# Kernel optimization log

Measured on AMD Instinct MI355X. Metric: run time of the kernel, lower is better.

## Reference

```python
import jax, jax.numpy as jnp
import numpy as np
import math

B, L, H, N2, NB = 16, 1024, 256, 64, 6
IN_DIM, OUT_DIM, STEP_EMB, NFEAT = 1, 1, 128, 4


def setup_inputs() -> dict:
    key = jax.random.key(0)
    ks = jax.random.split(key, 20)
    def rn(k, shape, s=0.02):
        return jax.random.normal(k, shape, dtype=jnp.float32) * s
    inp = {}
    inp["input"] = jax.random.normal(ks[0], (B, L, IN_DIM), dtype=jnp.float32)
    inp["t"] = jax.random.uniform(ks[1], (B,), dtype=jnp.float32) * 1000.0  # diffusion steps
    inp["features"] = jax.random.normal(ks[2], (B, L, NFEAT), dtype=jnp.float32)
    # input_init / time_init / output head (Linear weights stored (in,out))
    inp["W_in"] = rn(ks[3], (IN_DIM, H)); inp["b_in"] = jnp.zeros((H,), jnp.float32)
    inp["W_t1"] = rn(ks[4], (STEP_EMB, H)); inp["b_t1"] = jnp.zeros((H,), jnp.float32)
    inp["W_t2"] = rn(ks[5], (H, H)); inp["b_t2"] = jnp.zeros((H,), jnp.float32)
    inp["Wh1"] = rn(ks[6], (H, H)); inp["bh1"] = jnp.zeros((H,), jnp.float32)
    inp["Wh2"] = rn(ks[7], (H, OUT_DIM)); inp["bh2"] = jnp.zeros((OUT_DIM,), jnp.float32)
    # per-block params, stacked on leading NB axis
    inp["ln_g"] = jnp.ones((NB, H), jnp.float32); inp["ln_b"] = jnp.zeros((NB, H), jnp.float32)
    lo, hi = math.log(0.001), math.log(0.1)
    inp["log_dt"] = jax.random.uniform(ks[8], (NB, H), dtype=jnp.float32) * (hi - lo) + lo
    inp["A_re"] = 0.5 * jnp.ones((NB, H, N2), jnp.float32)  # A = -A_re + i*A_im (S4D-Lin)
    inp["A_im"] = jnp.broadcast_to(math.pi * jnp.arange(N2, dtype=jnp.float32), (NB, H, N2)) * jnp.ones((NB, H, N2), jnp.float32)
    inp["C_re"] = rn(ks[9], (NB, 2, H, N2), 0.7071)  # 2 = bidirectional channels
    inp["C_im"] = rn(ks[10], (NB, 2, H, N2), 0.7071)
    inp["D"] = rn(ks[11], (NB, H), 1.0)
    inp["Wo_s4"] = rn(ks[12], (NB, H, H)); inp["bo_s4"] = jnp.zeros((NB, H), jnp.float32)
    inp["Wt"] = rn(ks[13], (NB, H, H)); inp["bt"] = jnp.zeros((NB, H), jnp.float32)
    inp["W1"] = rn(ks[14], (NB, H, H)); inp["b1"] = jnp.zeros((NB, H), jnp.float32)
    inp["W2"] = rn(ks[15], (NB, H, H)); inp["b2"] = jnp.zeros((NB, H), jnp.float32)
    inp["Wf"] = rn(ks[16], (NB, NFEAT, H)); inp["bf"] = jnp.zeros((NB, H), jnp.float32)
    return inp


def _layernorm_ch(x, g, b, eps=1e-5):
    # x: (B,H,L); LayerNorm over channel dim H (torch applies it on (B,L,H))
    mu = x.mean(1, keepdims=True)
    v = ((x - mu) ** 2).mean(1, keepdims=True)
    return (x - mu) * jax.lax.rsqrt(v + eps) * g[None, :, None] + b[None, :, None]


def _s4(z, log_dt, A_re, A_im, C_re, C_im, D, Wo, bo):
    # Diagonal SSM (S4D) bidirectional convolution. z: (B,H,L)
    Lz = z.shape[-1]
    dt = jnp.exp(log_dt)                      # (H,)
    A = jax.lax.complex(-A_re, A_im)          # (H,N2)
    dtA = dt[:, None] * A                     # (H,N2)
    C = jax.lax.complex(C_re, C_im)           # (2,H,N2)
    Bt = C * (jnp.exp(dtA) - 1.0) / A         # ZOH discretization
    vand = jnp.exp(dtA[:, :, None] * jnp.arange(Lz, dtype=jnp.float32))  # (H,N2,L)
    K = 2.0 * jnp.real(jnp.einsum('chn,hnl->chl', Bt, vand))             # (2,H,L)
    zpad = jnp.zeros_like(K[0])
    k = jnp.concatenate([K[0], zpad], -1) + jnp.concatenate([zpad, K[1][:, ::-1]], -1)  # (H,2L)
    y = jnp.fft.irfft(jnp.fft.rfft(z, n=2 * Lz) * jnp.fft.rfft(k, n=2 * Lz), n=2 * Lz)[..., :Lz]
    y = y + z * D[:, None]
    y = jax.nn.gelu(y, approximate=False)
    return jnp.einsum('bhl,ho->bol', y, Wo) + bo[None, :, None]


def reference(input, t, features, W_in, b_in, W_t1, b_t1, W_t2, b_t2, Wh1, bh1, Wh2, bh2,
              ln_g, ln_b, log_dt, A_re, A_im, C_re, C_im, D, Wo_s4, bo_s4,
              Wt, bt, W1, b1, W2, b2, Wf, bf):
    x = jax.nn.relu(input @ W_in + b_in)                       # (B,L,H)
    half = W_t1.shape[0] // 2
    freqs = jnp.exp(jnp.arange(half, dtype=jnp.float32) * (-math.log(10000.0) / (half - 1)))
    ang = t[:, None] * freqs[None, :]
    temb = jnp.concatenate([jnp.sin(ang), jnp.cos(ang)], -1)   # (B,step_emb)
    temb = jax.nn.silu(temb @ W_t1 + b_t1)
    temb = jax.nn.silu(temb @ W_t2 + b_t2)                     # (B,H)
    x = jnp.swapaxes(x, 1, 2)                                  # (B,H,L)
    feat = jnp.swapaxes(features, 1, 2)                        # (B,F,L)
    skip = jnp.zeros_like(x)
    nb = ln_g.shape[0]
    for i in range(nb):
        tb = (temb @ Wt[i] + bt[i])[:, :, None]                # time_linear, broadcast over L
        u = x + tb
        z = _layernorm_ch(u, ln_g[i], ln_b[i])
        z = _s4(z, log_dt[i], A_re[i], A_im[i], C_re[i], C_im[i], D[i], Wo_s4[i], bo_s4[i])
        out = z + u                                            # S4Layer residual
        out = out + jnp.einsum('bfl,fh->bhl', feat, Wf[i]) + bf[i][None, :, None]
        g = jnp.tanh(out) * jax.nn.sigmoid(out)                # gated activation
        x = jnp.einsum('bhl,ho->bol', g, W1[i]) + b1[i][None, :, None] + x
        skip = skip + jnp.einsum('bhl,ho->bol', g, W2[i]) + b2[i][None, :, None]
    skip = jnp.swapaxes(skip, 1, 2)                            # (B,L,H)
    h = jax.nn.relu(skip @ Wh1 + bh1)
    return h @ Wh2 + bh2 + input
```

## Files before the change

kernel.cpp:

```cpp
#include <hip/hip_runtime.h>
#include <cmath>

constexpr int cB = 16, cL = 1024, cH = 256, cN = 64, cNB = 6, cNF = 4;
constexpr int cC = 8, cLc = cL / cC;
constexpr size_t SZ = (size_t)cB * cH * cL;

__global__ __launch_bounds__(256) void temb_kernel(
    const float* __restrict__ t, const float* __restrict__ Wt1, const float* __restrict__ bt1,
    const float* __restrict__ Wt2, const float* __restrict__ bt2,
    const float* __restrict__ Wt, const float* __restrict__ btb, float* __restrict__ tb) {
  __shared__ float e0[128], h1[256], h2[256];
  int b = blockIdx.x, tid = threadIdx.x;
  if (tid < 64) {
    float fr = expf((float)tid * (-logf(10000.0f) / 63.0f));
    float ang = t[b] * fr;
    e0[tid] = sinf(ang);
    e0[tid + 64] = cosf(ang);
  }
  __syncthreads();
  float a = bt1[tid];
  for (int k = 0; k < 128; ++k) a = fmaf(e0[k], Wt1[k * cH + tid], a);
  h1[tid] = a / (1.0f + expf(-a));
  __syncthreads();
  a = bt2[tid];
  for (int k = 0; k < 256; ++k) a = fmaf(h1[k], Wt2[k * cH + tid], a);
  h2[tid] = a / (1.0f + expf(-a));
  __syncthreads();
  for (int i = 0; i < cNB; ++i) {
    float acc = btb[i * cH + tid];
    const float* w = Wt + (size_t)i * cH * cH;
    for (int k = 0; k < 256; ++k) acc = fmaf(h2[k], w[k * cH + tid], acc);
    tb[((size_t)i * cB + b) * cH + tid] = acc;
  }
}

__global__ __launch_bounds__(256) void init_kernel(const float* __restrict__ inp,
    const float* __restrict__ Win, const float* __restrict__ bin,
    float* __restrict__ x, float* __restrict__ skip) {
  int idx = blockIdx.x * 256 + threadIdx.x;
  int l = idx & (cL - 1);
  int h = (idx >> 10) & (cH - 1);
  int b = idx >> 18;
  float v = fmaf(inp[b * cL + l], Win[h], bin[h]);
  x[idx] = v > 0.0f ? v : 0.0f;
  skip[idx] = 0.0f;
}

__global__ __launch_bounds__(256) void pre_ln_kernel(const float* __restrict__ x,
    const float* __restrict__ tb_all, const float* __restrict__ ln_g, const float* __restrict__ ln_b,
    float* __restrict__ z, int blk) {
  __shared__ float red[8][64];
  __shared__ float mur[64], rsr[64];
  int b = blockIdx.x >> 4;
  int l0 = (blockIdx.x & 15) << 6;
  int lq = threadIdx.x & 63, hq = threadIdx.x >> 6;
  int l = l0 + lq;
  const float* tb = tb_all + ((size_t)blk * cB + b) * cH;
  size_t base = ((size_t)b * cH + hq * 64) * cL + l;
  float s = 0.0f, s2 = 0.0f;
  for (int hh = 0; hh < 64; ++hh) {
    float v = x[base + (size_t)hh * cL] + tb[hq * 64 + hh];
    s += v;
    s2 = fmaf(v, v, s2);
  }
  red[hq][lq] = s;
  red[4 + hq][lq] = s2;
  __syncthreads();
  if (hq == 0) {
    float st = red[0][lq] + red[1][lq] + red[2][lq] + red[3][lq];
    float s2t = red[4][lq] + red[5][lq] + red[6][lq] + red[7][lq];
    float mu = st * (1.0f / cH);
    float var = s2t * (1.0f / cH) - mu * mu;
    mur[lq] = mu;
    rsr[lq] = rsqrtf(var + 1e-5f);
  }
  __syncthreads();
  float mu = mur[lq], r = rsr[lq];
  const float* g = ln_g + blk * cH;
  const float* be = ln_b + blk * cH;
  for (int hh = 0; hh < 64; ++hh) {
    int h = hq * 64 + hh;
    float v = (x[base + (size_t)hh * cL] + tb[h] - mu) * r;
    z[base + (size_t)hh * cL] = fmaf(v, g[h], be[h]);
  }
}

__global__ __launch_bounds__(256) void s4param_kernel(
    const float* __restrict__ logdt, const float* __restrict__ Are, const float* __restrict__ Aim,
    const float* __restrict__ Cre, const float* __restrict__ Cim,
    float4* __restrict__ P, float2* __restrict__ PW, int blk) {
  int idx = blockIdx.x * 256 + threadIdx.x;
  int n = idx & (cN - 1);
  int h = (idx >> 6) & (cH - 1);
  int dir = idx >> 14;
  float dt = expf(logdt[blk * cH + h]);
  float are = Are[((size_t)blk * cH + h) * cN + n];
  float aim = Aim[((size_t)blk * cH + h) * cN + n];
  float e = expf(-dt * are);
  float sn, cs;
  sincosf(dt * aim, &sn, &cs);
  float wr = e * cs, wi = e * sn;
  float inv = 1.0f / (are * are + aim * aim);
  float xr = wr - 1.0f, xi = wi;
  float tr = (xi * aim - xr * are) * inv;
  float ti = (-xr * aim - xi * are) * inv;
  float cr = Cre[(((size_t)blk * 2 + dir) * cH + h) * cN + n];
  float ci = Cim[(((size_t)blk * 2 + dir) * cH + h) * cN + n];
  float br = 2.0f * (cr * tr - ci * ti);
  float bi = 2.0f * (cr * ti + ci * tr);
  P[idx] = make_float4(wr, wi, br, bi);
  if (dir == 0) {
    float rr = wr, ri = wi;
#pragma unroll
    for (int q = 0; q < 7; ++q) {
      float nr = rr * rr - ri * ri;
      ri = 2.0f * rr * ri;
      rr = nr;
    }
    PW[h * cN + n] = make_float2(rr, ri);
  }
}

__global__ __launch_bounds__(256) void scanA1_kernel(const float* __restrict__ zb,
    const float4* __restrict__ P, float2* __restrict__ E) {
  int c = blockIdx.x, bh = blockIdx.y, dir = blockIdx.z;
  int b = bh >> 3, h0 = (bh & 7) << 5;
  int tid = threadIdx.x, wv = tid >> 6, lane = tid & 63;
  int hs = lane >> 3, j = lane & 7;
  int h = h0 + wv * 8 + hs;
  float wr[8], wi[8], sr[8], si[8];
  const float4* Ph = P + ((size_t)dir * cH + h) * cN + j * 8;
#pragma unroll
  for (int k = 0; k < 8; ++k) {
    float4 p4 = Ph[k];
    wr[k] = p4.x; wi[k] = p4.y;
    sr[k] = 0.0f; si[k] = 0.0f;
  }
  const float* zr = zb + ((size_t)b * cH + h) * cL;
  int c0 = c * cLc;
  if (dir == 0) {
    for (int m = 0; m < cLc / 4; ++m) {
      float4 z4 = *(const float4*)&zr[c0 + (m << 2)];
#pragma unroll
      for (int q = 0; q < 4; ++q) {
        float zv = q == 0 ? z4.x : q == 1 ? z4.y : q == 2 ? z4.z : z4.w;
#pragma unroll
        for (int k = 0; k < 8; ++k) {
          float nr = fmaf(wr[k], sr[k], zv);
          nr = fmaf(-wi[k], si[k], nr);
          float ni = wr[k] * si[k];
          ni = fmaf(wi[k], sr[k], ni);
          sr[k] = nr; si[k] = ni;
        }
      }
    }
  } else {
    for (int m = cLc / 4 - 1; m >= 0; --m) {
      float4 z4 = *(const float4*)&zr[c0 + (m << 2)];
#pragma unroll
      for (int q = 3; q >= 0; --q) {
        float zv = q == 0 ? z4.x : q == 1 ? z4.y : q == 2 ? z4.z : z4.w;
#pragma unroll
        for (int k = 0; k < 8; ++k) {
          float nr = fmaf(wr[k], sr[k], zv);
          nr = fmaf(-wi[k], si[k], nr);
          float ni = wr[k] * si[k];
          ni = fmaf(wi[k], sr[k], ni);
          sr[k] = nr; si[k] = ni;
        }
      }
    }
  }
  float2* Eo = E + ((((size_t)dir * cC + c) * cB + b) * cH + h) * cN + j * 8;
#pragma unroll
  for (int k = 0; k < 8; ++k) Eo[k] = make_float2(sr[k], si[k]);
}

__global__ __launch_bounds__(256) void scanA2_kernel(const float* __restrict__ zb,
    const float4* __restrict__ P, const float2* __restrict__ PW, const float2* __restrict__ E,
    float* __restrict__ yf, float* __restrict__ ybk) {
  int c = blockIdx.x, bh = blockIdx.y, dir = blockIdx.z;
  int b = bh >> 3, h0 = (bh & 7) << 5;
  int tid = threadIdx.x, wv = tid >> 6, lane = tid & 63;
  int hs = lane >> 3, j = lane & 7;
  int h = h0 + wv * 8 + hs;
  float sr[8] = {}, si[8] = {};
  {
    float qr[8], qi[8];
    const float2* PWh = PW + (size_t)h * cN + j * 8;
#pragma unroll
    for (int k = 0; k < 8; ++k) {
      float2 q2 = PWh[k];
      qr[k] = q2.x; qi[k] = q2.y;
    }
    const size_t cstride = (size_t)cB * cH * cN;
    const float2* Eb = E + (((size_t)dir * cC * cB + b) * cH + h) * cN + j * 8;
    if (dir == 0) {
      for (int cc = 0; cc < c; ++cc) {
        const float2* Ec = Eb + cc * cstride;
#pragma unroll
        for (int k = 0; k < 8; ++k) {
          float2 e2 = Ec[k];
          float t_r = fmaf(qr[k], sr[k], e2.x);
          t_r = fmaf(-qi[k], si[k], t_r);
          float t_i = fmaf(qr[k], si[k], e2.y);
          t_i = fmaf(qi[k], sr[k], t_i);
          sr[k] = t_r; si[k] = t_i;
        }
      }
    } else {
      for (int cc = cC - 1; cc > c; --cc) {
        const float2* Ec = Eb + cc * cstride;
#pragma unroll
        for (int k = 0; k < 8; ++k) {
          float2 e2 = Ec[k];
          float t_r = fmaf(qr[k], sr[k], e2.x);
          t_r = fmaf(-qi[k], si[k], t_r);
          float t_i = fmaf(qr[k], si[k], e2.y);
          t_i = fmaf(qi[k], sr[k], t_i);
          sr[k] = t_r; si[k] = t_i;
        }
      }
    }
  }
  float wr[8], wi[8], br[8], bi[8];
  const float4* Ph = P + ((size_t)dir * cH + h) * cN + j * 8;
#pragma unroll
  for (int k = 0; k < 8; ++k) {
    float4 p4 = Ph[k];
    wr[k] = p4.x; wi[k] = p4.y; br[k] = p4.z; bi[k] = p4.w;
  }
  const float* zr = zb + ((size_t)b * cH + h) * cL;
  int c0 = c * cLc;
  if (dir == 0) {
    float* yr = yf + ((size_t)b * cH + h) * cL;
    for (int m = 0; m < cLc / 4; ++m) {
      float4 z4 = *(const float4*)&zr[c0 + (m << 2)];
#pragma unroll
      for (int q = 0; q < 4; ++q) {
        float zv = q == 0 ? z4.x : q == 1 ? z4.y : q == 2 ? z4.z : z4.w;
        float p = 0.0f;
#pragma unroll
        for (int k = 0; k < 8; ++k) {
          float nr = fmaf(wr[k], sr[k], zv);
          nr = fmaf(-wi[k], si[k], nr);
          float ni = wr[k] * si[k];
          ni = fmaf(wi[k], sr[k], ni);
          sr[k] = nr; si[k] = ni;
          p = fmaf(br[k], nr, p);
          p = fmaf(-bi[k], ni, p);
        }
        p += __shfl_xor(p, 1);
        p += __shfl_xor(p, 2);
        p += __shfl_xor(p, 4);
        if (j == 0) yr[c0 + (m << 2) + q] = p;
      }
    }
  } else {
    float* yr = ybk + ((size_t)b * cH + h) * cL;
    for (int m = cLc / 4 - 1; m >= 0; --m) {
      float4 z4 = *(const float4*)&zr[c0 + (m << 2)];
#pragma unroll
      for (int q = 3; q >= 0; --q) {
        float zv = q == 0 ? z4.x : q == 1 ? z4.y : q == 2 ? z4.z : z4.w;
        float p = 0.0f;
#pragma unroll
        for (int k = 0; k < 8; ++k) {
          p = fmaf(br[k], sr[k], p);
          p = fmaf(-bi[k], si[k], p);
        }
        p += __shfl_xor(p, 1);
        p += __shfl_xor(p, 2);
        p += __shfl_xor(p, 4);
        if (j == 0) yr[c0 + (m << 2) + q] = p;
#pragma unroll
        for (int k = 0; k < 8; ++k) {
          float nr = fmaf(wr[k], sr[k], zv);
          nr = fmaf(-wi[k], si[k], nr);
          float ni = wr[k] * si[k];
          ni = fmaf(wi[k], sr[k], ni);
          sr[k] = nr; si[k] = ni;
        }
      }
    }
  }
}

__global__ __launch_bounds__(256) void scan_kernel(
    const float* __restrict__ zb, const float* __restrict__ log_dt,
    const float* __restrict__ A_re, const float* __restrict__ A_im,
    const float* __restrict__ C_re, const float* __restrict__ C_im,
    float* __restrict__ yf, float* __restrict__ ybk, int blk) {
  int dir = blockIdx.y;
  int b = blockIdx.x >> 3;
  int h0 = (blockIdx.x & 7) << 5;
  int tid = threadIdx.x;
  int wv = tid >> 6, lane = tid & 63;
  int hs = lane >> 3, j = lane & 7;
  int h = h0 + wv * 8 + hs;
  float dt = expf(log_dt[blk * cH + h]);
  const float* Ar = A_re + ((size_t)blk * cH + h) * cN;
  const float* Ai = A_im + ((size_t)blk * cH + h) * cN;
  const float* Cr = C_re + (((size_t)blk * 2 + dir) * cH + h) * cN;
  const float* Ci = C_im + (((size_t)blk * 2 + dir) * cH + h) * cN;
  float wr[8], wi[8], br[8], bi[8], sr[8], si[8];
#pragma unroll
  for (int k = 0; k < 8; ++k) {
    int n = j * 8 + k;
    float are = Ar[n], aim = Ai[n];
    float e = expf(-dt * are);
    float sn, cs;
    sincosf(dt * aim, &sn, &cs);
    float w_r = e * cs, w_i = e * sn;
    float inv = 1.0f / (are * are + aim * aim);
    float xr = w_r - 1.0f, xi = w_i;
    float tr = (xi * aim - xr * are) * inv;
    float ti = (-xr * aim - xi * are) * inv;
    float cr = Cr[n], ci = Ci[n];
    br[k] = 2.0f * (cr * tr - ci * ti);
    bi[k] = 2.0f * (cr * ti + ci * tr);
    wr[k] = w_r; wi[k] = w_i;
    sr[k] = 0.0f; si[k] = 0.0f;
  }
  const float* zr = zb + ((size_t)b * cH + h) * cL;
  if (dir == 0) {
    float* yr = yf + ((size_t)b * cH + h) * cL;
    for (int l = 0; l < cL; ++l) {
      float zv = zr[l];
      float p = 0.0f;
#pragma unroll
      for (int k = 0; k < 8; ++k) {
        float nr = fmaf(wr[k], sr[k], zv);
        nr = fmaf(-wi[k], si[k], nr);
        float ni = wr[k] * si[k];
        ni = fmaf(wi[k], sr[k], ni);
        sr[k] = nr; si[k] = ni;
        p = fmaf(br[k], nr, p);
        p = fmaf(-bi[k], ni, p);
      }
      p += __shfl_xor(p, 1);
      p += __shfl_xor(p, 2);
      p += __shfl_xor(p, 4);
      if (j == 0) yr[l] = p;
    }
  } else {
    float* yr = ybk + ((size_t)b * cH + h) * cL;
    for (int l = cL - 1; l >= 0; --l) {
      float p = 0.0f;
#pragma unroll
      for (int k = 0; k < 8; ++k) {
        p = fmaf(br[k], sr[k], p);
        p = fmaf(-bi[k], si[k], p);
      }
      p += __shfl_xor(p, 1);
      p += __shfl_xor(p, 2);
      p += __shfl_xor(p, 4);
      if (j == 0) yr[l] = p;
      float zv = zr[l];
#pragma unroll
      for (int k = 0; k < 8; ++k) {
        float nr = fmaf(wr[k], sr[k], zv);
        nr = fmaf(-wi[k], si[k], nr);
        float ni = wr[k] * si[k];
        ni = fmaf(wi[k], sr[k], ni);
        sr[k] = nr; si[k] = ni;
      }
    }
  }
}

__global__ __launch_bounds__(256) void gelu_kernel(const float* __restrict__ y2,
    const float* __restrict__ zz, const float* __restrict__ Dp, float* __restrict__ y1io, int blk) {
  int idx = blockIdx.x * 256 + threadIdx.x;
  int h = (idx >> 10) & (cH - 1);
  float v = y1io[idx] + y2[idx] + zz[idx] * Dp[blk * cH + h];
  y1io[idx] = 0.5f * v * (1.0f + erff(v * 0.70710678118654752f));
}

#define GEMM_CORE(WPTR)                                                          \
  int l0 = blockIdx.x * 128, o0 = blockIdx.y * 64, b = blockIdx.z;               \
  int tid = threadIdx.x;                                                         \
  int tx = tid & 15, ty = tid >> 4;                                              \
  const float* Gb = G + (size_t)b * cH * cL;                                     \
  float acc[4][8] = {};                                                          \
  {                                                                              \
    int ar = tid >> 6, ac = tid & 63;                                            \
    int brr = tid >> 7, bc = tid & 127;                                          \
    for (int kk = 0; kk < cH; kk += 16) {                                        \
      _Pragma("unroll")                                                          \
      for (int rr = 0; rr < 4; ++rr)                                             \
        As[ar + rr * 4][ac] = (WPTR)[(size_t)(kk + ar + rr * 4) * cH + o0 + ac]; \
      _Pragma("unroll")                                                          \
      for (int rr = 0; rr < 8; ++rr)                                             \
        Bs[brr + rr * 2][bc] = Gb[(size_t)(kk + brr + rr * 2) * cL + l0 + bc];   \
      __syncthreads();                                                           \
      _Pragma("unroll")                                                          \
      for (int k = 0; k < 16; ++k) {                                             \
        const float4 av = *(const float4*)&As[k][ty << 2];                       \
        const float4 b0 = *(const float4*)&Bs[k][tx << 3];                       \
        const float4 b1 = *(const float4*)&Bs[k][(tx << 3) + 4];                 \
        FMA8(0, av.x) FMA8(1, av.y) FMA8(2, av.z) FMA8(3, av.w)                  \
      }                                                                          \
      __syncthreads();                                                           \
    }                                                                            \
  }

#define FMA8(oi, aw)                                     \
  acc[oi][0] = fmaf(aw, b0.x, acc[oi][0]);               \
  acc[oi][1] = fmaf(aw, b0.y, acc[oi][1]);               \
  acc[oi][2] = fmaf(aw, b0.z, acc[oi][2]);               \
  acc[oi][3] = fmaf(aw, b0.w, acc[oi][3]);               \
  acc[oi][4] = fmaf(aw, b1.x, acc[oi][4]);               \
  acc[oi][5] = fmaf(aw, b1.y, acc[oi][5]);               \
  acc[oi][6] = fmaf(aw, b1.z, acc[oi][6]);               \
  acc[oi][7] = fmaf(aw, b1.w, acc[oi][7]);

__global__ __launch_bounds__(256) void gemm_act_kernel(const float* __restrict__ W,
    const float* __restrict__ bo, const float* __restrict__ G,
    const float* __restrict__ x, const float* __restrict__ tb_all,
    const float* __restrict__ features, const float* __restrict__ Wf,
    const float* __restrict__ bfb, float* __restrict__ C, int blk) {
  __shared__ float As[16][64];
  __shared__ float Bs[16][128];
  GEMM_CORE(W)
  int lbase = l0 + (tx << 3);
  float4 fv[8];
#pragma unroll
  for (int li = 0; li < 8; ++li)
    fv[li] = *(const float4*)&features[((size_t)b * cL + lbase + li) * cNF];
  const float* Wfi = Wf + (size_t)blk * cNF * cH;
  const float* tb = tb_all + ((size_t)blk * cB + b) * cH;
#pragma unroll
  for (int oi = 0; oi < 4; ++oi) {
    int oo = o0 + (ty << 2) + oi;
    float wf0 = Wfi[oo], wf1 = Wfi[cH + oo], wf2 = Wfi[2 * cH + oo], wf3 = Wfi[3 * cH + oo];
    float bb = bo[oo] + bfb[blk * cH + oo] + tb[oo];
    size_t row = ((size_t)b * cH + oo) * cL + lbase;
    const float4 x0 = *(const float4*)&x[row];
    const float4 x1 = *(const float4*)&x[row + 4];
    float xv[8] = {x0.x, x0.y, x0.z, x0.w, x1.x, x1.y, x1.z, x1.w};
    float out[8];
#pragma unroll
    for (int li = 0; li < 8; ++li) {
      float v = acc[oi][li] + bb + xv[li];
      v = fmaf(fv[li].x, wf0, v);
      v = fmaf(fv[li].y, wf1, v);
      v = fmaf(fv[li].z, wf2, v);
      v = fmaf(fv[li].w, wf3, v);
      float tv = tanhf(v);
      float sv = 1.0f / (1.0f + expf(-v));
      out[li] = tv * sv;
    }
    *(float4*)&C[row] = make_float4(out[0], out[1], out[2], out[3]);
    *(float4*)&C[row + 4] = make_float4(out[4], out[5], out[6], out[7]);
  }
}

__global__ __launch_bounds__(256) void gemm_dual_kernel(const float* __restrict__ W1,
    const float* __restrict__ b1, const float* __restrict__ W2, const float* __restrict__ b2,
    const float* __restrict__ G, float* __restrict__ xio, float* __restrict__ skio) {
  __shared__ float As[16][64];
  __shared__ float As2[16][64];
  __shared__ float Bs[16][128];
  int l0 = blockIdx.x * 128, o0 = blockIdx.y * 64, b = blockIdx.z;
  int tid = threadIdx.x;
  int tx = tid & 15, ty = tid >> 4;
  const float* Gb = G + (size_t)b * cH * cL;
  float acc[4][8] = {};
  float acc2[4][8] = {};
  {
    int ar = tid >> 6, ac = tid & 63;
    int brr = tid >> 7, bc = tid & 127;
    for (int kk = 0; kk < cH; kk += 16) {
#pragma unroll
      for (int rr = 0; rr < 4; ++rr) {
        As[ar + rr * 4][ac] = W1[(size_t)(kk + ar + rr * 4) * cH + o0 + ac];
        As2[ar + rr * 4][ac] = W2[(size_t)(kk + ar + rr * 4) * cH + o0 + ac];
      }
#pragma unroll
      for (int rr = 0; rr < 8; ++rr)
        Bs[brr + rr * 2][bc] = Gb[(size_t)(kk + brr + rr * 2) * cL + l0 + bc];
      __syncthreads();
#pragma unroll
      for (int k = 0; k < 16; ++k) {
        const float4 b0 = *(const float4*)&Bs[k][tx << 3];
        const float4 b1v = *(const float4*)&Bs[k][(tx << 3) + 4];
        {
          const float4 av = *(const float4*)&As[k][ty << 2];
#define FMA8D(AC, oi, aw)                          \
  AC[oi][0] = fmaf(aw, b0.x, AC[oi][0]);           \
  AC[oi][1] = fmaf(aw, b0.y, AC[oi][1]);           \
  AC[oi][2] = fmaf(aw, b0.z, AC[oi][2]);           \
  AC[oi][3] = fmaf(aw, b0.w, AC[oi][3]);           \
  AC[oi][4] = fmaf(aw, b1v.x, AC[oi][4]);          \
  AC[oi][5] = fmaf(aw, b1v.y, AC[oi][5]);          \
  AC[oi][6] = fmaf(aw, b1v.z, AC[oi][6]);          \
  AC[oi][7] = fmaf(aw, b1v.w, AC[oi][7]);
          FMA8D(acc, 0, av.x) FMA8D(acc, 1, av.y) FMA8D(acc, 2, av.z) FMA8D(acc, 3, av.w)
        }
        {
          const float4 av = *(const float4*)&As2[k][ty << 2];
          FMA8D(acc2, 0, av.x) FMA8D(acc2, 1, av.y) FMA8D(acc2, 2, av.z) FMA8D(acc2, 3, av.w)
        }
      }
      __syncthreads();
    }
  }
  int lbase = l0 + (tx << 3);
#pragma unroll
  for (int oi = 0; oi < 4; ++oi) {
    int oo = o0 + (ty << 2) + oi;
    float bb1 = b1[oo], bb2 = b2[oo];
    size_t row = ((size_t)b * cH + oo) * cL + lbase;
    float4 xv0 = *(const float4*)&xio[row];
    float4 xv1 = *(const float4*)&xio[row + 4];
    float4 sv0 = *(const float4*)&skio[row];
    float4 sv1 = *(const float4*)&skio[row + 4];
    xv0.x += acc[oi][0] + bb1; xv0.y += acc[oi][1] + bb1;
    xv0.z += acc[oi][2] + bb1; xv0.w += acc[oi][3] + bb1;
    xv1.x += acc[oi][4] + bb1; xv1.y += acc[oi][5] + bb1;
    xv1.z += acc[oi][6] + bb1; xv1.w += acc[oi][7] + bb1;
    sv0.x += acc2[oi][0] + bb2; sv0.y += acc2[oi][1] + bb2;
    sv0.z += acc2[oi][2] + bb2; sv0.w += acc2[oi][3] + bb2;
    sv1.x += acc2[oi][4] + bb2; sv1.y += acc2[oi][5] + bb2;
    sv1.z += acc2[oi][6] + bb2; sv1.w += acc2[oi][7] + bb2;
    *(float4*)&xio[row] = xv0;
    *(float4*)&xio[row + 4] = xv1;
    *(float4*)&skio[row] = sv0;
    *(float4*)&skio[row + 4] = sv1;
  }
}

__global__ __launch_bounds__(256) void gemm_relu_kernel(const float* __restrict__ W,
    const float* __restrict__ bias, const float* __restrict__ G, float* __restrict__ C) {
  __shared__ float As[16][64];
  __shared__ float Bs[16][128];
  GEMM_CORE(W)
  int lbase = l0 + (tx << 3);
#pragma unroll
  for (int oi = 0; oi < 4; ++oi) {
    int oo = o0 + (ty << 2) + oi;
    float bb = bias[oo];
    size_t row = ((size_t)b * cH + oo) * cL + lbase;
    float4 v0, v1;
    v0.x = fmaxf(acc[oi][0] + bb, 0.0f); v0.y = fmaxf(acc[oi][1] + bb, 0.0f);
    v0.z = fmaxf(acc[oi][2] + bb, 0.0f); v0.w = fmaxf(acc[oi][3] + bb, 0.0f);
    v1.x = fmaxf(acc[oi][4] + bb, 0.0f); v1.y = fmaxf(acc[oi][5] + bb, 0.0f);
    v1.z = fmaxf(acc[oi][6] + bb, 0.0f); v1.w = fmaxf(acc[oi][7] + bb, 0.0f);
    *(float4*)&C[row] = v0;
    *(float4*)&C[row + 4] = v1;
  }
}

__global__ __launch_bounds__(256) void head_kernel(const float* __restrict__ hb,
    const float* __restrict__ Wh2, const float* __restrict__ bh2,
    const float* __restrict__ inp, float* __restrict__ out) {
  int idx = blockIdx.x * 256 + threadIdx.x;
  int b = idx >> 10, l = idx & (cL - 1);
  float acc = bh2[0] + inp[idx];
  const float* hr = hb + (size_t)b * cH * cL + l;
  for (int o = 0; o < cH; ++o) acc = fmaf(hr[(size_t)o * cL], Wh2[o], acc);
  out[idx] = acc;
}

extern "C" void kernel_launch(void* const* d_in, const int* in_sizes, int n_in,
                              void* d_out, int out_size, void* d_ws, size_t ws_size,
                              hipStream_t stream) {
  const float* input = (const float*)d_in[0];
  const float* t     = (const float*)d_in[1];
  const float* feats = (const float*)d_in[2];
  const float* W_in  = (const float*)d_in[3];
  const float* b_in  = (const float*)d_in[4];
  const float* W_t1  = (const float*)d_in[5];
  const float* b_t1  = (const float*)d_in[6];
  const float* W_t2  = (const float*)d_in[7];
  const float* b_t2  = (const float*)d_in[8];
  const float* Wh1   = (const float*)d_in[9];
  const float* bh1   = (const float*)d_in[10];
  const float* Wh2   = (const float*)d_in[11];
  const float* bh2   = (const float*)d_in[12];
  const float* ln_g  = (const float*)d_in[13];
  const float* ln_b  = (const float*)d_in[14];
  const float* logdt = (const float*)d_in[15];
  const float* A_re  = (const float*)d_in[16];
  const float* A_im  = (const float*)d_in[17];
  const float* C_re  = (const float*)d_in[18];
  const float* C_im  = (const float*)d_in[19];
  const float* Dp    = (const float*)d_in[20];
  const float* Wo_s4 = (const float*)d_in[21];
  const float* bo_s4 = (const float*)d_in[22];
  const float* Wt    = (const float*)d_in[23];
  const float* bt_   = (const float*)d_in[24];
  const float* W1    = (const float*)d_in[25];
  const float* b1    = (const float*)d_in[26];
  const float* W2    = (const float*)d_in[27];
  const float* b2    = (const float*)d_in[28];
  const float* Wf    = (const float*)d_in[29];
  const float* bf_   = (const float*)d_in[30];

  float* ws = (float*)d_ws;
  float* xb   = ws;
  float* skb  = ws + SZ;
  float* zbuf = ws + 2 * SZ;
  float* yb   = ws + 3 * SZ;
  float* y2b  = ws + 4 * SZ;
  float* tbb  = ws + 5 * SZ;
  size_t off = 5 * SZ + 32768;
  float4* Pbuf = (float4*)(ws + off);
  float2* PWb  = (float2*)(ws + off + 131072);
  float2* Ebuf = (float2*)(ws + off + 131072 + 32768);
  const size_t NEED = (off + 131072 + 32768 + (size_t)2 * cC * cB * cH * cN * 2) * 4;
  const bool chunked = ws_size >= NEED;

  dim3 ggrid(cL / 128, cH / 64, cB);
  dim3 sgrid(cC, cB * (cH / 32), 2);

  temb_kernel<<<cB, 256, 0, stream>>>(t, W_t1, b_t1, W_t2, b_t2, Wt, bt_, tbb);
  init_kernel<<<(int)(SZ / 256), 256, 0, stream>>>(input, W_in, b_in, xb, skb);

  for (int i = 0; i < cNB; ++i) {
    pre_ln_kernel<<<cB * (cL / 64), 256, 0, stream>>>(xb, tbb, ln_g, ln_b, zbuf, i);
    if (chunked) {
      s4param_kernel<<<128, 256, 0, stream>>>(logdt, A_re, A_im, C_re, C_im, Pbuf, PWb, i);
      scanA1_kernel<<<sgrid, 256, 0, stream>>>(zbuf, Pbuf, Ebuf);
      scanA2_kernel<<<sgrid, 256, 0, stream>>>(zbuf, Pbuf, PWb, Ebuf, yb, y2b);
    } else {
      scan_kernel<<<dim3(cB * (cH / 32), 2), 256, 0, stream>>>(zbuf, logdt, A_re, A_im, C_re, C_im, yb, y2b, i);
    }
    gelu_kernel<<<(int)(SZ / 256), 256, 0, stream>>>(y2b, zbuf, Dp, yb, i);
    gemm_act_kernel<<<ggrid, 256, 0, stream>>>(
        Wo_s4 + (size_t)i * cH * cH, bo_s4 + i * cH, yb, xb, tbb, feats, Wf, bf_, zbuf, i);
    gemm_dual_kernel<<<ggrid, 256, 0, stream>>>(
        W1 + (size_t)i * cH * cH, b1 + i * cH, W2 + (size_t)i * cH * cH, b2 + i * cH,
        zbuf, xb, skb);
  }

  gemm_relu_kernel<<<ggrid, 256, 0, stream>>>(Wh1, bh1, skb, yb);
  head_kernel<<<(cB * cL) / 256, 256, 0, stream>>>(yb, Wh2, bh2, input, (float*)d_out);
}
```

Measured before the change: 1.942 ms.

## Fuse bidirectional scan passes, add inter-chunk carry kernel, fold D-skip and GELU into scan

Each scan kernel now handles both directions in one block instead of splitting them over a grid z-dimension. A new scanB kernel propagates chunk carries once and stores exclusive prefix states in place, so scanA2 no longer recomputes the serial chunk recurrence per chunk. scanA2 adds both directions' outputs in LDS, applies the D skip term and GELU, and writes y directly, which removes the y2 buffer and the separate gelu kernel. In exchange there are half as many scan blocks (less parallelism), an extra small kernel launch, and more LDS use per block.

```diff
diff --git a/kernel.cpp b/kernel.cpp
--- a/kernel.cpp
+++ b/kernel.cpp
@@ -4,6 +4,10 @@
 constexpr int cB = 16, cL = 1024, cH = 256, cN = 64, cNB = 6, cNF = 4;
 constexpr int cC = 8, cLc = cL / cC;
 constexpr size_t SZ = (size_t)cB * cH * cL;
+
+__device__ __forceinline__ float gelu_f(float v) {
+  return 0.5f * v * (1.0f + erff(v * 0.70710678118654752f));
+}
 
 __global__ __launch_bounds__(256) void temb_kernel(
     const float* __restrict__ t, const float* __restrict__ Wt1, const float* __restrict__ bt1,
@@ -123,22 +127,18 @@
 
 __global__ __launch_bounds__(256) void scanA1_kernel(const float* __restrict__ zb,
     const float4* __restrict__ P, float2* __restrict__ E) {
-  int c = blockIdx.x, bh = blockIdx.y, dir = blockIdx.z;
+  int c = blockIdx.x, bh = blockIdx.y;
   int b = bh >> 3, h0 = (bh & 7) << 5;
   int tid = threadIdx.x, wv = tid >> 6, lane = tid & 63;
   int hs = lane >> 3, j = lane & 7;
   int h = h0 + wv * 8 + hs;
-  float wr[8], wi[8], sr[8], si[8];
-  const float4* Ph = P + ((size_t)dir * cH + h) * cN + j * 8;
-#pragma unroll
-  for (int k = 0; k < 8; ++k) {
-    float4 p4 = Ph[k];
-    wr[k] = p4.x; wi[k] = p4.y;
-    sr[k] = 0.0f; si[k] = 0.0f;
-  }
   const float* zr = zb + ((size_t)b * cH + h) * cL;
   int c0 = c * cLc;
-  if (dir == 0) {
+  {
+    float wr[8], wi[8], sr[8] = {}, si[8] = {};
+    const float4* Ph = P + (size_t)h * cN + j * 8;
+#pragma unroll
+    for (int k = 0; k < 8; ++k) { float4 p4 = Ph[k]; wr[k] = p4.x; wi[k] = p4.y; }
     for (int m = 0; m < cLc / 4; ++m) {
       float4 z4 = *(const float4*)&zr[c0 + (m << 2)];
 #pragma unroll
@@ -154,7 +154,15 @@
         }
       }
     }
-  } else {
+    float2* Eo = E + ((((size_t)0 * cC + c) * cB + b) * cH + h) * cN + j * 8;
+#pragma unroll
+    for (int k = 0; k < 8; ++k) Eo[k] = make_float2(sr[k], si[k]);
+  }
+  {
+    float wr[8], wi[8], sr[8] = {}, si[8] = {};
+    const float4* Ph = P + ((size_t)cH + h) * cN + j * 8;
+#pragma unroll
+    for (int k = 0; k < 8; ++k) { float4 p4 = Ph[k]; wr[k] = p4.x; wi[k] = p4.y; }
     for (int m = cLc / 4 - 1; m >= 0; --m) {
       float4 z4 = *(const float4*)&zr[c0 + (m << 2)];
 #pragma unroll
@@ -170,70 +178,66 @@
         }
       }
     }
-  }
-  float2* Eo = E + ((((size_t)dir * cC + c) * cB + b) * cH + h) * cN + j * 8;
-#pragma unroll
-  for (int k = 0; k < 8; ++k) Eo[k] = make_float2(sr[k], si[k]);
+    float2* Eo = E + ((((size_t)cC + c) * cB + b) * cH + h) * cN + j * 8;
+#pragma unroll
+    for (int k = 0; k < 8; ++k) Eo[k] = make_float2(sr[k], si[k]);
+  }
+}
+
+__global__ __launch_bounds__(256) void scanB_kernel(float2* __restrict__ E,
+    const float2* __restrict__ PW) {
+  int idx = blockIdx.x * 256 + threadIdx.x;
+  int n = idx & (cN - 1);
+  int h = (idx >> 6) & (cH - 1);
+  int b = (idx >> 14) & (cB - 1);
+  int dir = idx >> 18;
+  float2 q2 = PW[h * cN + n];
+  float qr = q2.x, qi = q2.y;
+  const size_t cs = (size_t)cB * cH * cN;
+  size_t e0 = ((((size_t)dir * cC) * cB + b) * cH + h) * cN + n;
+  float sr = 0.0f, si = 0.0f;
+  if (dir == 0) {
+    for (int cc = 0; cc < cC; ++cc) {
+      float2 e = E[e0 + cc * cs];
+      E[e0 + cc * cs] = make_float2(sr, si);
+      float nr = fmaf(qr, sr, e.x); nr = fmaf(-qi, si, nr);
+      float ni = fmaf(qr, si, e.y); ni = fmaf(qi, sr, ni);
+      sr = nr; si = ni;
+    }
+  } else {
+    for (int cc = cC - 1; cc >= 0; --cc) {
+      float2 e = E[e0 + cc * cs];
+      E[e0 + cc * cs] = make_float2(sr, si);
+      float nr = fmaf(qr, sr, e.x); nr = fmaf(-qi, si, nr);
+      float ni = fmaf(qr, si, e.y); ni = fmaf(qi, sr, ni);
+      sr = nr; si = ni;
+    }
+  }
 }
 
 __global__ __launch_bounds__(256) void scanA2_kernel(const float* __restrict__ zb,
-    const float4* __restrict__ P, const float2* __restrict__ PW, const float2* __restrict__ E,
-    float* __restrict__ yf, float* __restrict__ ybk) {
-  int c = blockIdx.x, bh = blockIdx.y, dir = blockIdx.z;
+    const float4* __restrict__ P, const float2* __restrict__ E, const float* __restrict__ Dp,
+    float* __restrict__ y, int blk) {
+  __shared__ float acc_lds[32][cLc + 1];
+  int c = blockIdx.x, bh = blockIdx.y;
   int b = bh >> 3, h0 = (bh & 7) << 5;
   int tid = threadIdx.x, wv = tid >> 6, lane = tid & 63;
   int hs = lane >> 3, j = lane & 7;
-  int h = h0 + wv * 8 + hs;
-  float sr[8] = {}, si[8] = {};
-  {
-    float qr[8], qi[8];
-    const float2* PWh = PW + (size_t)h * cN + j * 8;
-#pragma unroll
-    for (int k = 0; k < 8; ++k) {
-      float2 q2 = PWh[k];
-      qr[k] = q2.x; qi[k] = q2.y;
-    }
-    const size_t cstride = (size_t)cB * cH * cN;
-    const float2* Eb = E + (((size_t)dir * cC * cB + b) * cH + h) * cN + j * 8;
-    if (dir == 0) {
-      for (int cc = 0; cc < c; ++cc) {
-        const float2* Ec = Eb + cc * cstride;
-#pragma unroll
-        for (int k = 0; k < 8; ++k) {
-          float2 e2 = Ec[k];
-          float t_r = fmaf(qr[k], sr[k], e2.x);
-          t_r = fmaf(-qi[k], si[k], t_r);
-          float t_i = fmaf(qr[k], si[k], e2.y);
-          t_i = fmaf(qi[k], sr[k], t_i);
-          sr[k] = t_r; si[k] = t_i;
-        }
-      }
-    } else {
-      for (int cc = cC - 1; cc > c; --cc) {
-        const float2* Ec = Eb + cc * cstride;
-#pragma unroll
-        for (int k = 0; k < 8; ++k) {
-          float2 e2 = Ec[k];
-          float t_r = fmaf(qr[k], sr[k], e2.x);
-          t_r = fmaf(-qi[k], si[k], t_r);
-          float t_i = fmaf(qr[k], si[k], e2.y);
-          t_i = fmaf(qi[k], sr[k], t_i);
-          sr[k] = t_r; si[k] = t_i;
-        }
-      }
-    }
-  }
-  float wr[8], wi[8], br[8], bi[8];
-  const float4* Ph = P + ((size_t)dir * cH + h) * cN + j * 8;
-#pragma unroll
-  for (int k = 0; k < 8; ++k) {
-    float4 p4 = Ph[k];
-    wr[k] = p4.x; wi[k] = p4.y; br[k] = p4.z; bi[k] = p4.w;
-  }
+  int lch = wv * 8 + hs;
+  int h = h0 + lch;
   const float* zr = zb + ((size_t)b * cH + h) * cL;
   int c0 = c * cLc;
-  if (dir == 0) {
-    float* yr = yf + ((size_t)b * cH + h) * cL;
+  {
+    float wr[8], wi[8], br[8], bi[8], sr[8], si[8];
+    const float4* Ph = P + (size_t)h * cN + j * 8;
+    const float2* Cc = E + ((((size_t)0 * cC + c) * cB + b) * cH + h) * cN + j * 8;
+#pragma unroll
+    for (int k = 0; k < 8; ++k) {
+      float4 p4 = Ph[k];
+      wr[k] = p4.x; wi[k] = p4.y; br[k] = p4.z; bi[k] = p4.w;
+      float2 e2 = Cc[k];
+      sr[k] = e2.x; si[k] = e2.y;
+    }
     for (int m = 0; m < cLc / 4; ++m) {
       float4 z4 = *(const float4*)&zr[c0 + (m << 2)];
 #pragma unroll
@@ -253,11 +257,21 @@
         p += __shfl_xor(p, 1);
         p += __shfl_xor(p, 2);
         p += __shfl_xor(p, 4);
-        if (j == 0) yr[c0 + (m << 2) + q] = p;
-      }
-    }
-  } else {
-    float* yr = ybk + ((size_t)b * cH + h) * cL;
+        if (j == 0) acc_lds[lch][(m << 2) + q] = p;
+      }
+    }
+  }
+  {
+    float wr[8], wi[8], br[8], bi[8], sr[8], si[8];
+    const float4* Ph = P + ((size_t)cH + h) * cN + j * 8;
+    const float2* Cc = E + ((((size_t)cC + c) * cB + b) * cH + h) * cN + j * 8;
+#pragma unroll
+    for (int k = 0; k < 8; ++k) {
+      float4 p4 = Ph[k];
+      wr[k] = p4.x; wi[k] = p4.y; br[k] = p4.z; bi[k] = p4.w;
+      float2 e2 = Cc[k];
+      sr[k] = e2.x; si[k] = e2.y;
+    }
     for (int m = cLc / 4 - 1; m >= 0; --m) {
       float4 z4 = *(const float4*)&zr[c0 + (m << 2)];
 #pragma unroll
@@ -272,7 +286,7 @@
         p += __shfl_xor(p, 1);
         p += __shfl_xor(p, 2);
         p += __shfl_xor(p, 4);
-        if (j == 0) yr[c0 + (m << 2) + q] = p;
+        if (j == 0) acc_lds[lch][(m << 2) + q] += p;
 #pragma unroll
         for (int k = 0; k < 8; ++k) {
           float nr = fmaf(wr[k], sr[k], zv);
@@ -283,6 +297,23 @@
         }
       }
     }
+  }
+  __syncthreads();
+  int lc2 = tid >> 3, part = tid & 7;
+  int hh = h0 + lc2;
+  float Dv = Dp[blk * cH + hh];
+  const float* zrow = zb + ((size_t)b * cH + hh) * cL + c0;
+  float* yrow = y + ((size_t)b * cH + hh) * cL + c0;
+#pragma unroll
+  for (int g = 0; g < 4; ++g) {
+    int l = part * 16 + g * 4;
+    float4 z4 = *(const float4*)&zrow[l];
+    float4 o;
+    o.x = gelu_f(acc_lds[lc2][l + 0] + z4.x * Dv);
+    o.y = gelu_f(acc_lds[lc2][l + 1] + z4.y * Dv);
+    o.z = gelu_f(acc_lds[lc2][l + 2] + z4.z * Dv);
+    o.w = gelu_f(acc_lds[lc2][l + 3] + z4.w * Dv);
+    *(float4*)&yrow[l] = o;
   }
 }
 
@@ -374,7 +405,7 @@
   int idx = blockIdx.x * 256 + threadIdx.x;
   int h = (idx >> 10) & (cH - 1);
   float v = y1io[idx] + y2[idx] + zz[idx] * Dp[blk * cH + h];
-  y1io[idx] = 0.5f * v * (1.0f + erff(v * 0.70710678118654752f));
+  y1io[idx] = gelu_f(v);
 }
 
 #define GEMM_CORE(WPTR)                                                          \
@@ -613,7 +644,7 @@
   const bool chunked = ws_size >= NEED;
 
   dim3 ggrid(cL / 128, cH / 64, cB);
-  dim3 sgrid(cC, cB * (cH / 32), 2);
+  dim3 sgrid(cC, cB * (cH / 32));
 
   temb_kernel<<<cB, 256, 0, stream>>>(t, W_t1, b_t1, W_t2, b_t2, Wt, bt_, tbb);
   init_kernel<<<(int)(SZ / 256), 256, 0, stream>>>(input, W_in, b_in, xb, skb);
@@ -623,11 +654,12 @@
     if (chunked) {
       s4param_kernel<<<128, 256, 0, stream>>>(logdt, A_re, A_im, C_re, C_im, Pbuf, PWb, i);
       scanA1_kernel<<<sgrid, 256, 0, stream>>>(zbuf, Pbuf, Ebuf);
-      scanA2_kernel<<<sgrid, 256, 0, stream>>>(zbuf, Pbuf, PWb, Ebuf, yb, y2b);
+      scanB_kernel<<<2048, 256, 0, stream>>>(Ebuf, PWb);
+      scanA2_kernel<<<sgrid, 256, 0, stream>>>(zbuf, Pbuf, Ebuf, Dp, yb, i);
     } else {
       scan_kernel<<<dim3(cB * (cH / 32), 2), 256, 0, stream>>>(zbuf, logdt, A_re, A_im, C_re, C_im, yb, y2b, i);
-    }
-    gelu_kernel<<<(int)(SZ / 256), 256, 0, stream>>>(y2b, zbuf, Dp, yb, i);
+      gelu_kernel<<<(int)(SZ / 256), 256, 0, stream>>>(y2b, zbuf, Dp, yb, i);
+    }
     gemm_act_kernel<<<ggrid, 256, 0, stream>>>(
         Wo_s4 + (size_t)i * cH * cH, bo_s4 + i * cH, yb, xb, tbb, feats, Wf, bf_, zbuf, i);
     gemm_dual_kernel<<<ggrid, 256, 0, stream>>>(
```

Result: no change. 1.932 ms (-0.5%).
